# Kernel tuning notes

Hardware: AMD Instinct MI355X
Metric: run time of the kernel (lower is better)

Reference implementation:

```python
import jax, jax.numpy as jnp
import numpy as np

ALPHA = 0.2          # LeakyReLU negative slope
NEG_INF = -9e15      # mask fill value, matches torch source
ADJ_EPS = 1e-6       # clamp min for log(adj)


def setup_inputs() -> dict:
    key = jax.random.key(0)
    k1, k2, k3, k4, k5 = jax.random.split(key, 5)
    N, F_IN, H, D = 4096, 256, 4, 64  # out_features = H*D = 256
    h = jax.random.normal(k1, (N, F_IN), dtype=jnp.float32)
    # xavier_uniform-ish scale for W (gain 1.414)
    limW = 1.414 * np.sqrt(6.0 / (F_IN + D))
    W = jax.random.uniform(k2, (H, F_IN, D), dtype=jnp.float32, minval=-limW, maxval=limW)
    lima = 1.414 * np.sqrt(6.0 / (D + 1))
    a_src = jax.random.uniform(k3, (H, D, 1), dtype=jnp.float32, minval=-lima, maxval=lima)
    a_dst = jax.random.uniform(k4, (H, D, 1), dtype=jnp.float32, minval=-lima, maxval=lima)
    # random 0/1 dense adjacency (float, as the torch module takes log(adj))
    adj = jax.random.randint(k5, (N, N), 0, 2).astype(jnp.float32)
    return {"h": h, "adj": adj, "W": W, "a_src": a_src, "a_dst": a_dst}


def reference(h, adj, W, a_src, a_dst):
    N = h.shape[0]
    # Wh: (H, N, D)
    Wh = jnp.einsum('ni,hid->hnd', h, W)
    # per-node source/dest scores: (H, N, 1)
    attn_src = jnp.einsum('hnd,hdo->hno', Wh, a_src)
    attn_dst = jnp.einsum('hnd,hdo->hno', Wh, a_dst)
    # broadcast to dense (H, N, N) logits
    e = jax.nn.leaky_relu(attn_src + jnp.swapaxes(attn_dst, -1, -2), negative_slope=ALPHA)
    adj_b = adj[None]  # (1, N, N)
    attention = jnp.where(adj_b > 0, e + jnp.log(jnp.maximum(adj_b, ADJ_EPS)), NEG_INF)
    attention = jax.nn.softmax(attention, axis=-1)
    # dropout p=0.0 (eval) -> identity
    h_prime = jnp.einsum('hnm,hmd->hnd', attention, Wh)        # (H, N, D)
    h_prime = jnp.transpose(h_prime, (1, 0, 2)).reshape(N, -1)  # (N, H*D)
    return jax.nn.elu(h_prime)  # concat=True branch
```

## Files before the change

kernel.cpp:

```cpp
#include <hip/hip_runtime.h>

typedef __attribute__((ext_vector_type(4))) float f32x4;
typedef __attribute__((ext_vector_type(8))) short short8;
typedef __attribute__((ext_vector_type(8))) __bf16 bf16x8;

constexpr int kN = 4096;
constexpr int kF = 256;
constexpr int kH = 4;
constexpr int kD = 64;
constexpr int kMP = 264;
constexpr float kLog2e = 1.4426950408889634f;

__device__ __forceinline__ unsigned short f2us(float x) {
  __bf16 b = (__bf16)x;
  return __builtin_bit_cast(unsigned short, b);
}

__global__ __launch_bounds__(256) void k_wh(const float* __restrict__ hmat,
                                            const float* __restrict__ W,
                                            const float* __restrict__ a_src,
                                            const float* __restrict__ a_dst,
                                            unsigned short* __restrict__ whb,
                                            float* __restrict__ s_src,
                                            float* __restrict__ s_dst,
                                            float* __restrict__ pmax) {
  const int h = blockIdx.x & 3, rb = blockIdx.x >> 2;
  const int row0 = rb * 64;
  const int t = threadIdx.x;
  __shared__ unsigned short wlds[16384];
  __shared__ float bm[4];
  {
    const int d = t & 63;
    const int dt = d >> 4, dl = d & 15;
    for (int kb = 0; kb < 64; kb++) {
      const int k = kb * 4 + (t >> 6);
      const float wv = W[((size_t)h * kF + k) * kD + d];
      const int ks = k >> 5, kl = k & 31;
      const int lane2 = ((kl >> 3) << 4) | dl;
      const int e = kl & 7;
      wlds[(((ks * 4 + dt) * 64 + lane2) << 3) + e] = f2us(wv);
    }
  }
  __syncthreads();
  const int wave = t >> 6, lane = t & 63;
  const int lr = lane & 15, lg = lane >> 4;
  const int nrow = row0 + wave * 16 + lr;
  f32x4 acc[4] = {};
  const float* hrow = hmat + (size_t)nrow * kF + 8 * lg;
#pragma unroll
  for (int ks = 0; ks < 8; ks++) {
    const f32x4 h0 = *reinterpret_cast<const f32x4*>(hrow + ks * 32);
    const f32x4 h1 = *reinterpret_cast<const f32x4*>(hrow + ks * 32 + 4);
    bf16x8 af;
#pragma unroll
    for (int j = 0; j < 4; j++) { af[j] = (__bf16)h0[j]; af[4 + j] = (__bf16)h1[j]; }
#pragma unroll
    for (int dt = 0; dt < 4; dt++) {
      const short8 bs = *reinterpret_cast<const short8*>(wlds + (((ks * 4 + dt) * 64 + lane) << 3));
      acc[dt] = __builtin_amdgcn_mfma_f32_16x16x32_bf16(af, __builtin_bit_cast(bf16x8, bs), acc[dt], 0, 0, 0);
    }
  }
#pragma unroll
  for (int dt = 0; dt < 4; dt++) {
#pragma unroll
    for (int r = 0; r < 4; r++) {
      const int n = row0 + wave * 16 + lg * 4 + r;
      const int mstep = n >> 5, kl = n & 31;
      const int lane2 = ((kl >> 3) << 4) | lr;
      const int e = kl & 7;
      whb[((((size_t)(h * 128 + mstep) * 4 + dt) * 64 + lane2) << 3) + e] = f2us(acc[dt][r]);
    }
  }
  float as4[4], ad4[4];
#pragma unroll
  for (int dt = 0; dt < 4; dt++) {
    as4[dt] = a_src[h * kD + dt * 16 + lr];
    ad4[dt] = a_dst[h * kD + dt * 16 + lr];
  }
  float wmax = -1e30f;
#pragma unroll
  for (int r = 0; r < 4; r++) {
    float ps = acc[0][r] * as4[0] + acc[1][r] * as4[1] + acc[2][r] * as4[2] + acc[3][r] * as4[3];
    float pd = acc[0][r] * ad4[0] + acc[1][r] * ad4[1] + acc[2][r] * ad4[2] + acc[3][r] * ad4[3];
#pragma unroll
    for (int off = 1; off < 16; off <<= 1) {
      ps += __shfl_xor(ps, off);
      pd += __shfl_xor(pd, off);
    }
    const int n = row0 + wave * 16 + lg * 4 + r;
    if (lr == 0) { s_src[h * kN + n] = ps; s_dst[h * kN + n] = pd; }
    wmax = fmaxf(wmax, pd);
  }
  wmax = fmaxf(wmax, __shfl_xor(wmax, 16));
  wmax = fmaxf(wmax, __shfl_xor(wmax, 32));
  if (lane == 0) bm[wave] = wmax;
  __syncthreads();
  if (t == 0)
    pmax[blockIdx.x] = fmaxf(fmaxf(bm[0], bm[1]), fmaxf(bm[2], bm[3]));
}

__device__ __forceinline__ bf16x8 make_p2(const f32x4 E1a, const f32x4 E1b,
                                          const f32x4 E2a, const f32x4 E2b,
                                          const float K1, const float K2,
                                          const unsigned int m) {
  bf16x8 r;
#pragma unroll
  for (int j = 0; j < 4; j++) {
    const float pv = fmaxf(E1a[j] * K1, E2a[j] * K2);
    r[j] = (__bf16)((m & (1u << j)) ? pv : 0.0f);
  }
#pragma unroll
  for (int j = 0; j < 4; j++) {
    const float pv = fmaxf(E1b[j] * K1, E2b[j] * K2);
    r[4 + j] = (__bf16)((m & (16u << j)) ? pv : 0.0f);
  }
  return r;
}

__global__ __launch_bounds__(512, 4) void k_attn(const float* __restrict__ adj,
                                                 const unsigned short* __restrict__ whb,
                                                 const float* __restrict__ s_src,
                                                 const float* __restrict__ s_dst,
                                                 const float* __restrict__ pmax,
                                                 float* __restrict__ accP,
                                                 float* __restrict__ zP) {
  const int bid = blockIdx.x;
  const int rb = bid >> 2, cs = bid & 3;
  const int row0 = rb * 32;
  const int colbase = cs * 1024;
  const int t = threadIdx.x;
  const int wave = t >> 6, lane = t & 63;
  const int h = wave & 3, q = wave >> 2;
  const int lr = lane & 15, lg = lane >> 4;

  __shared__ float el1[4][1024];
  __shared__ float el2[4][1024];
  __shared__ unsigned char lmaskB[16 * kMP];
  __shared__ float zx[4][32];

  {
    f32x4 v[16];
    const float* abase = adj + (size_t)(row0 + wave * 4) * kN + colbase;
#pragma unroll
    for (int j = 0; j < 4; j++)
#pragma unroll
      for (int p = 0; p < 4; p++) {
        const int off = ((p >> 1) << 9) + 8 * lane + ((p & 1) << 2);
        v[j * 4 + p] = *reinterpret_cast<const f32x4*>(abase + (size_t)j * kN + off);
      }
#pragma unroll
    for (int j = 0; j < 4; j++) {
      const int rl = wave * 4 + j;
#pragma unroll
      for (int half = 0; half < 2; half++) {
        unsigned int b = 0;
#pragma unroll
        for (int i = 0; i < 4; i++) {
          b |= (v[j * 4 + half * 2][i] != 0.0f ? 1u : 0u) << i;
          b |= (v[j * 4 + half * 2 + 1][i] != 0.0f ? 1u : 0u) << (4 + i);
        }
        const int o = half * 64 + lane;
        lmaskB[(o >> 3) * kMP + rl * 8 + (o & 7)] = (unsigned char)b;
      }
    }
  }

#pragma unroll
  for (int j = 0; j < 2; j++) {
    const int idx = t + j * 512;
    const int hh = idx >> 8, c4 = (idx & 255) * 4;
    const f32x4 sd = *reinterpret_cast<const f32x4*>(s_dst + hh * kN + colbase + c4);
    f32x4 e1, e2;
#pragma unroll
    for (int i = 0; i < 4; i++) {
      const float u = sd[i] * kLog2e;
      e1[i] = __builtin_amdgcn_exp2f(u);
      e2[i] = __builtin_amdgcn_exp2f(0.2f * u);
    }
    *reinterpret_cast<f32x4*>(&el1[hh][c4]) = e1;
    *reinterpret_cast<f32x4*>(&el2[hh][c4]) = e2;
  }

  float M = pmax[(lane << 2) | h];
#pragma unroll
  for (int off = 1; off < 64; off <<= 1) M = fmaxf(M, __shfl_xor(M, off));

  float K1[2], K2[2];
#pragma unroll
  for (int rt = 0; rt < 2; rt++) {
    const float A = s_src[h * kN + row0 + rt * 16 + lr];
    const float xb = A + M;
    const float B = fmaxf(xb, 0.2f * xb);
    K1[rt] = __builtin_amdgcn_exp2f((A - B) * kLog2e);
    K2[rt] = __builtin_amdgcn_exp2f((0.2f * A - B) * kLog2e);
  }

  __syncthreads();

  const int Boff = (q << 2) | lg;
  unsigned int cw0[4], cw1[4];
#pragma unroll
  for (int w = 0; w < 4; w++) {
    unsigned int a0 = 0, a1 = 0;
#pragma unroll
    for (int d = 0; d < 4; d++) {
      const int c = w * 4 + d;
      a0 |= (unsigned int)lmaskB[c * kMP + lr * 8 + Boff] << (8 * d);
      a1 |= (unsigned int)lmaskB[c * kMP + (lr + 16) * 8 + Boff] << (8 * d);
    }
    cw0[w] = a0; cw1[w] = a1;
  }

  f32x4 acc0[4] = {}, acc1[4] = {};
  f32x4 accz0 = {}, accz1 = {};
  bf16x8 ones;
#pragma unroll
  for (int e = 0; e < 8; e++) ones[e] = (__bf16)1.0f;

  const float* e1p = &el1[h][q * 32 + 8 * lg];
  const float* e2p = &el2[h][q * 32 + 8 * lg];
  const short8* wb = reinterpret_cast<const short8*>(whb) + (size_t)h * 32768 + lane;
  const int mstep0 = cs * 32 + q;

  short8 bw[2][4];
#pragma unroll
  for (int s = 0; s < 2; s++) {
    const short8* p = wb + (size_t)(mstep0 + s * 2) * 256;
    bw[s][0] = p[0]; bw[s][1] = p[64]; bw[s][2] = p[128]; bw[s][3] = p[192];
  }

#define UNIT(ITC, CM0, CM1)                                                    \
  {                                                                            \
    const short8 cb0 = bw[(ITC) & 1][0], cb1 = bw[(ITC) & 1][1],               \
                 cb2 = bw[(ITC) & 1][2], cb3 = bw[(ITC) & 1][3];               \
    const short8* pp = wb + (size_t)(mstep0 + ((ITC) + 2) * 2) * 256;          \
    bw[(ITC) & 1][0] = pp[0];                                                  \
    bw[(ITC) & 1][1] = pp[64];                                                 \
    bw[(ITC) & 1][2] = pp[128];                                                \
    bw[(ITC) & 1][3] = pp[192];                                                \
    const f32x4 E1a = *reinterpret_cast<const f32x4*>(e1p + (ITC) * 64);       \
    const f32x4 E1b = *reinterpret_cast<const f32x4*>(e1p + (ITC) * 64 + 4);   \
    const f32x4 E2a = *reinterpret_cast<const f32x4*>(e2p + (ITC) * 64);       \
    const f32x4 E2b = *reinterpret_cast<const f32x4*>(e2p + (ITC) * 64 + 4);   \
    const bf16x8 P0 = make_p2(E1a, E1b, E2a, E2b, K1[0], K2[0], (CM0));        \
    const bf16x8 P1 = make_p2(E1a, E1b, E2a, E2b, K1[1], K2[1], (CM1));        \
    const bf16x8 B0 = __builtin_bit_cast(bf16x8, cb0);                         \
    const bf16x8 B1 = __builtin_bit_cast(bf16x8, cb1);                         \
    const bf16x8 B2 = __builtin_bit_cast(bf16x8, cb2);                         \
    const bf16x8 B3 = __builtin_bit_cast(bf16x8, cb3);                         \
    acc0[0] = __builtin_amdgcn_mfma_f32_16x16x32_bf16(P0, B0, acc0[0], 0, 0, 0); \
    acc1[0] = __builtin_amdgcn_mfma_f32_16x16x32_bf16(P1, B0, acc1[0], 0, 0, 0); \
    acc0[1] = __builtin_amdgcn_mfma_f32_16x16x32_bf16(P0, B1, acc0[1], 0, 0, 0); \
    acc1[1] = __builtin_amdgcn_mfma_f32_16x16x32_bf16(P1, B1, acc1[1], 0, 0, 0); \
    acc0[2] = __builtin_amdgcn_mfma_f32_16x16x32_bf16(P0, B2, acc0[2], 0, 0, 0); \
    acc1[2] = __builtin_amdgcn_mfma_f32_16x16x32_bf16(P1, B2, acc1[2], 0, 0, 0); \
    acc0[3] = __builtin_amdgcn_mfma_f32_16x16x32_bf16(P0, B3, acc0[3], 0, 0, 0); \
    acc1[3] = __builtin_amdgcn_mfma_f32_16x16x32_bf16(P1, B3, acc1[3], 0, 0, 0); \
    accz0 = __builtin_amdgcn_mfma_f32_16x16x32_bf16(P0, ones, accz0, 0, 0, 0); \
    accz1 = __builtin_amdgcn_mfma_f32_16x16x32_bf16(P1, ones, accz1, 0, 0, 0); \
  }

#pragma unroll
  for (int it = 0; it < 16; ++it) {
    const unsigned cm0 = (cw0[it >> 2] >> ((it & 3) * 8)) & 0xFFu;
    const unsigned cm1 = (cw1[it >> 2] >> ((it & 3) * 8)) & 0xFFu;
    UNIT(it, cm0, cm1);
  }
#undef UNIT

  __syncthreads();
  if (q == 1) {
#pragma unroll
    for (int dt = 0; dt < 4; dt++) {
      *reinterpret_cast<f32x4*>(&el1[h][(dt * 64 + lane) * 4]) = acc0[dt];
      *reinterpret_cast<f32x4*>(&el2[h][(dt * 64 + lane) * 4]) = acc1[dt];
    }
    if (lr == 0) {
#pragma unroll
      for (int r = 0; r < 4; r++) {
        zx[h][lg * 4 + r] = accz0[r];
        zx[h][16 + lg * 4 + r] = accz1[r];
      }
    }
  }
  __syncthreads();
  if (q == 0) {
#pragma unroll
    for (int dt = 0; dt < 4; dt++) {
      acc0[dt] += *reinterpret_cast<const f32x4*>(&el1[h][(dt * 64 + lane) * 4]);
      acc1[dt] += *reinterpret_cast<const f32x4*>(&el2[h][(dt * 64 + lane) * 4]);
    }
    const size_t ob = ((size_t)(cs * 4 + h) * kN + row0) * kD;
#pragma unroll
    for (int dt = 0; dt < 4; dt++)
#pragma unroll
      for (int r = 0; r < 4; r++) {
        accP[ob + (size_t)(lg * 4 + r) * kD + dt * 16 + lr] = acc0[dt][r];
        accP[ob + (size_t)(16 + lg * 4 + r) * kD + dt * 16 + lr] = acc1[dt][r];
      }
    if (lr == 0) {
      const size_t zb = (size_t)(cs * 4 + h) * kN + row0;
#pragma unroll
      for (int r = 0; r < 4; r++) {
        zP[zb + lg * 4 + r] = accz0[r] + zx[h][lg * 4 + r];
        zP[zb + 16 + lg * 4 + r] = accz1[r] + zx[h][16 + lg * 4 + r];
      }
    }
  }
}

__global__ __launch_bounds__(256) void k_fin(const float* __restrict__ accP,
                                             const float* __restrict__ zP,
                                             float* __restrict__ out) {
  const int idx = blockIdx.x * 256 + threadIdx.x;
  const int d4 = idx & 15;
  const int hh = (idx >> 4) & 3;
  const int n = idx >> 6;
  f32x4 v = {};
  float z = 0.0f;
#pragma unroll
  for (int s = 0; s < 4; s++) {
    v += reinterpret_cast<const f32x4*>(accP)[((size_t)(s * 4 + hh) * kN + n) * 16 + d4];
    z += zP[(size_t)(s * 4 + hh) * kN + n];
  }
  const float rz = 1.0f / z;
  f32x4 o;
#pragma unroll
  for (int j = 0; j < 4; j++) {
    const float x = v[j] * rz;
    o[j] = x > 0.0f ? x : (__builtin_amdgcn_exp2f(x * kLog2e) - 1.0f);
  }
  reinterpret_cast<f32x4*>(out)[(size_t)n * 64 + hh * 16 + d4] = o;
}

extern "C" void kernel_launch(void* const* d_in, const int* in_sizes, int n_in,
                              void* d_out, int out_size, void* d_ws, size_t ws_size,
                              hipStream_t stream) {
  const float* hmat  = (const float*)d_in[0];
  const float* adj   = (const float*)d_in[1];
  const float* W     = (const float*)d_in[2];
  const float* a_src = (const float*)d_in[3];
  const float* a_dst = (const float*)d_in[4];
  float* out = (float*)d_out;

  char* ws = (char*)d_ws;
  unsigned short* whb = (unsigned short*)(ws);
  float* s_src  = (float*)(ws + 0x200000);
  float* s_dst  = (float*)(ws + 0x210000);
  float* pmax   = (float*)(ws + 0x220000);
  float* accP   = (float*)(ws + 0x240000);
  float* zP     = (float*)(ws + 0x1240000);

  hipLaunchKernelGGL(k_wh, dim3(256), dim3(256), 0, stream,
                     hmat, W, a_src, a_dst, whb, s_src, s_dst, pmax);
  hipLaunchKernelGGL(k_attn, dim3(512), dim3(512), 0, stream,
                     adj, whb, s_src, s_dst, pmax, accP, zP);
  hipLaunchKernelGGL(k_fin, dim3(1024), dim3(256), 0, stream, accP, zP, out);
}
```

Baseline: 51.32 us.

## Split attention column chunk across four wave groups with 1024-thread blocks

Doubles k_attn block size to 1024 threads so each head's 1024-column chunk is split across four wave groups instead of two. Each wave does half the MFMA iterations, adj mask loading is spread over more waves, and partial accumulators are combined through an extra two-level LDS reduction. It also replaces the conditional mask select with a bitwise AND mask. This adds shared memory (an extra 32KB buffer), more barriers and register-pressure limits under launch_bounds(1024,8), in exchange for more latency hiding per CU.

Result: slower. 121.6 us (+137.0%).

```diff
diff --git a/kernel.cpp b/kernel.cpp
--- a/kernel.cpp
+++ b/kernel.cpp
@@ -99,31 +99,32 @@
     pmax[blockIdx.x] = fmaxf(fmaxf(bm[0], bm[1]), fmaxf(bm[2], bm[3]));
 }
 
+__device__ __forceinline__ float msel(float pv, unsigned m, int j) {
+  const unsigned keep = (unsigned)(-(int)((m >> j) & 1u));
+  return __builtin_bit_cast(float, __builtin_bit_cast(unsigned, pv) & keep);
+}
+
 __device__ __forceinline__ bf16x8 make_p2(const f32x4 E1a, const f32x4 E1b,
                                           const f32x4 E2a, const f32x4 E2b,
                                           const float K1, const float K2,
                                           const unsigned int m) {
   bf16x8 r;
 #pragma unroll
-  for (int j = 0; j < 4; j++) {
-    const float pv = fmaxf(E1a[j] * K1, E2a[j] * K2);
-    r[j] = (__bf16)((m & (1u << j)) ? pv : 0.0f);
-  }
-#pragma unroll
-  for (int j = 0; j < 4; j++) {
-    const float pv = fmaxf(E1b[j] * K1, E2b[j] * K2);
-    r[4 + j] = (__bf16)((m & (16u << j)) ? pv : 0.0f);
-  }
+  for (int j = 0; j < 4; j++)
+    r[j] = (__bf16)msel(fmaxf(E1a[j] * K1, E2a[j] * K2), m, j);
+#pragma unroll
+  for (int j = 0; j < 4; j++)
+    r[4 + j] = (__bf16)msel(fmaxf(E1b[j] * K1, E2b[j] * K2), m, 4 + j);
   return r;
 }
 
-__global__ __launch_bounds__(512, 4) void k_attn(const float* __restrict__ adj,
-                                                 const unsigned short* __restrict__ whb,
-                                                 const float* __restrict__ s_src,
-                                                 const float* __restrict__ s_dst,
-                                                 const float* __restrict__ pmax,
-                                                 float* __restrict__ accP,
-                                                 float* __restrict__ zP) {
+__global__ __launch_bounds__(1024, 8) void k_attn(const float* __restrict__ adj,
+                                                  const unsigned short* __restrict__ whb,
+                                                  const float* __restrict__ s_src,
+                                                  const float* __restrict__ s_dst,
+                                                  const float* __restrict__ pmax,
+                                                  float* __restrict__ accP,
+                                                  float* __restrict__ zP) {
   const int bid = blockIdx.x;
   const int rb = bid >> 2, cs = bid & 3;
   const int row0 = rb * 32;
@@ -135,22 +136,23 @@
 
   __shared__ float el1[4][1024];
   __shared__ float el2[4][1024];
+  __shared__ float cb2[4][2048];
   __shared__ unsigned char lmaskB[16 * kMP];
-  __shared__ float zx[4][32];
+  __shared__ float zxA[4][32], zxB[4][32];
 
   {
-    f32x4 v[16];
-    const float* abase = adj + (size_t)(row0 + wave * 4) * kN + colbase;
-#pragma unroll
-    for (int j = 0; j < 4; j++)
+    f32x4 v[8];
+    const float* abase = adj + (size_t)(row0 + wave * 2) * kN + colbase;
+#pragma unroll
+    for (int j = 0; j < 2; j++)
 #pragma unroll
       for (int p = 0; p < 4; p++) {
         const int off = ((p >> 1) << 9) + 8 * lane + ((p & 1) << 2);
         v[j * 4 + p] = *reinterpret_cast<const f32x4*>(abase + (size_t)j * kN + off);
       }
 #pragma unroll
-    for (int j = 0; j < 4; j++) {
-      const int rl = wave * 4 + j;
+    for (int j = 0; j < 2; j++) {
+      const int rl = wave * 2 + j;
 #pragma unroll
       for (int half = 0; half < 2; half++) {
         unsigned int b = 0;
@@ -165,10 +167,8 @@
     }
   }
 
-#pragma unroll
-  for (int j = 0; j < 2; j++) {
-    const int idx = t + j * 512;
-    const int hh = idx >> 8, c4 = (idx & 255) * 4;
+  {
+    const int hh = t >> 8, c4 = (t & 255) * 4;
     const f32x4 sd = *reinterpret_cast<const f32x4*>(s_dst + hh * kN + colbase + c4);
     f32x4 e1, e2;
 #pragma unroll
@@ -197,19 +197,17 @@
 
   __syncthreads();
 
-  const int Boff = (q << 2) | lg;
-  unsigned int cw0[4], cw1[4];
-#pragma unroll
-  for (int w = 0; w < 4; w++) {
-    unsigned int a0 = 0, a1 = 0;
+  const int g = 4 * q + lg;
+  const int base_c = g >> 3, s = g & 7;
+  unsigned int cw0[2] = {0, 0}, cw1[2] = {0, 0};
+#pragma unroll
+  for (int w = 0; w < 2; w++)
 #pragma unroll
     for (int d = 0; d < 4; d++) {
-      const int c = w * 4 + d;
-      a0 |= (unsigned int)lmaskB[c * kMP + lr * 8 + Boff] << (8 * d);
-      a1 |= (unsigned int)lmaskB[c * kMP + (lr + 16) * 8 + Boff] << (8 * d);
-    }
-    cw0[w] = a0; cw1[w] = a1;
-  }
+      const int c = base_c + 8 * w + 2 * d;
+      cw0[w] |= (unsigned int)lmaskB[c * kMP + lr * 8 + s] << (8 * d);
+      cw1[w] |= (unsigned int)lmaskB[c * kMP + (lr + 16) * 8 + s] << (8 * d);
+    }
 
   f32x4 acc0[4] = {}, acc1[4] = {};
   f32x4 accz0 = {}, accz1 = {};
@@ -224,29 +222,29 @@
 
   short8 bw[2][4];
 #pragma unroll
-  for (int s = 0; s < 2; s++) {
-    const short8* p = wb + (size_t)(mstep0 + s * 2) * 256;
-    bw[s][0] = p[0]; bw[s][1] = p[64]; bw[s][2] = p[128]; bw[s][3] = p[192];
+  for (int sx = 0; sx < 2; sx++) {
+    const short8* p = wb + (size_t)(mstep0 + sx * 4) * 256;
+    bw[sx][0] = p[0]; bw[sx][1] = p[64]; bw[sx][2] = p[128]; bw[sx][3] = p[192];
   }
 
 #define UNIT(ITC, CM0, CM1)                                                    \
   {                                                                            \
     const short8 cb0 = bw[(ITC) & 1][0], cb1 = bw[(ITC) & 1][1],               \
-                 cb2 = bw[(ITC) & 1][2], cb3 = bw[(ITC) & 1][3];               \
-    const short8* pp = wb + (size_t)(mstep0 + ((ITC) + 2) * 2) * 256;          \
+                 cb2r = bw[(ITC) & 1][2], cb3 = bw[(ITC) & 1][3];              \
+    const short8* pp = wb + (size_t)(mstep0 + ((ITC) + 2) * 4) * 256;          \
     bw[(ITC) & 1][0] = pp[0];                                                  \
     bw[(ITC) & 1][1] = pp[64];                                                 \
     bw[(ITC) & 1][2] = pp[128];                                                \
     bw[(ITC) & 1][3] = pp[192];                                                \
-    const f32x4 E1a = *reinterpret_cast<const f32x4*>(e1p + (ITC) * 64);       \
-    const f32x4 E1b = *reinterpret_cast<const f32x4*>(e1p + (ITC) * 64 + 4);   \
-    const f32x4 E2a = *reinterpret_cast<const f32x4*>(e2p + (ITC) * 64);       \
-    const f32x4 E2b = *reinterpret_cast<const f32x4*>(e2p + (ITC) * 64 + 4);   \
+    const f32x4 E1a = *reinterpret_cast<const f32x4*>(e1p + (ITC) * 128);      \
+    const f32x4 E1b = *reinterpret_cast<const f32x4*>(e1p + (ITC) * 128 + 4);  \
+    const f32x4 E2a = *reinterpret_cast<const f32x4*>(e2p + (ITC) * 128);      \
+    const f32x4 E2b = *reinterpret_cast<const f32x4*>(e2p + (ITC) * 128 + 4);  \
     const bf16x8 P0 = make_p2(E1a, E1b, E2a, E2b, K1[0], K2[0], (CM0));        \
     const bf16x8 P1 = make_p2(E1a, E1b, E2a, E2b, K1[1], K2[1], (CM1));        \
     const bf16x8 B0 = __builtin_bit_cast(bf16x8, cb0);                         \
     const bf16x8 B1 = __builtin_bit_cast(bf16x8, cb1);                         \
-    const bf16x8 B2 = __builtin_bit_cast(bf16x8, cb2);                         \
+    const bf16x8 B2 = __builtin_bit_cast(bf16x8, cb2r);                        \
     const bf16x8 B3 = __builtin_bit_cast(bf16x8, cb3);                         \
     acc0[0] = __builtin_amdgcn_mfma_f32_16x16x32_bf16(P0, B0, acc0[0], 0, 0, 0); \
     acc1[0] = __builtin_amdgcn_mfma_f32_16x16x32_bf16(P1, B0, acc1[0], 0, 0, 0); \
@@ -261,7 +259,7 @@
   }
 
 #pragma unroll
-  for (int it = 0; it < 16; ++it) {
+  for (int it = 0; it < 8; ++it) {
     const unsigned cm0 = (cw0[it >> 2] >> ((it & 3) * 8)) & 0xFFu;
     const unsigned cm1 = (cw1[it >> 2] >> ((it & 3) * 8)) & 0xFFu;
     UNIT(it, cm0, cm1);
@@ -275,13 +273,59 @@
       *reinterpret_cast<f32x4*>(&el1[h][(dt * 64 + lane) * 4]) = acc0[dt];
       *reinterpret_cast<f32x4*>(&el2[h][(dt * 64 + lane) * 4]) = acc1[dt];
     }
-    if (lr == 0) {
+    if (lr == 0)
 #pragma unroll
       for (int r = 0; r < 4; r++) {
-        zx[h][lg * 4 + r] = accz0[r];
-        zx[h][16 + lg * 4 + r] = accz1[r];
-      }
-    }
+        zxA[h][lg * 4 + r] = accz0[r];
+        zxA[h][16 + lg * 4 + r] = accz1[r];
+      }
+  }
+  if (q == 3) {
+#pragma unroll
+    for (int dt = 0; dt < 4; dt++) {
+      *reinterpret_cast<f32x4*>(&cb2[h][(dt * 64 + lane) * 4]) = acc0[dt];
+      *reinterpret_cast<f32x4*>(&cb2[h][1024 + (dt * 64 + lane) * 4]) = acc1[dt];
+    }
+    if (lr == 0)
+#pragma unroll
+      for (int r = 0; r < 4; r++) {
+        zxB[h][lg * 4 + r] = accz0[r];
+        zxB[h][16 + lg * 4 + r] = accz1[r];
+      }
+  }
+  __syncthreads();
+  if (q == 0) {
+#pragma unroll
+    for (int dt = 0; dt < 4; dt++) {
+      acc0[dt] += *reinterpret_cast<const f32x4*>(&el1[h][(dt * 64 + lane) * 4]);
+      acc1[dt] += *reinterpret_cast<const f32x4*>(&el2[h][(dt * 64 + lane) * 4]);
+    }
+  }
+  if (q == 2) {
+#pragma unroll
+    for (int dt = 0; dt < 4; dt++) {
+      acc0[dt] += *reinterpret_cast<const f32x4*>(&cb2[h][(dt * 64 + lane) * 4]);
+      acc1[dt] += *reinterpret_cast<const f32x4*>(&cb2[h][1024 + (dt * 64 + lane) * 4]);
+    }
+#pragma unroll
+    for (int r = 0; r < 4; r++) {
+      accz0[r] += zxB[h][lg * 4 + r];
+      accz1[r] += zxB[h][16 + lg * 4 + r];
+    }
+  }
+  __syncthreads();
+  if (q == 2) {
+#pragma unroll
+    for (int dt = 0; dt < 4; dt++) {
+      *reinterpret_cast<f32x4*>(&el1[h][(dt * 64 + lane) * 4]) = acc0[dt];
+      *reinterpret_cast<f32x4*>(&el2[h][(dt * 64 + lane) * 4]) = acc1[dt];
+    }
+    if (lr == 0)
+#pragma unroll
+      for (int r = 0; r < 4; r++) {
+        zxB[h][lg * 4 + r] = accz0[r];
+        zxB[h][16 + lg * 4 + r] = accz1[r];
+      }
   }
   __syncthreads();
   if (q == 0) {
@@ -302,8 +346,9 @@
       const size_t zb = (size_t)(cs * 4 + h) * kN + row0;
 #pragma unroll
       for (int r = 0; r < 4; r++) {
-        zP[zb + lg * 4 + r] = accz0[r] + zx[h][lg * 4 + r];
-        zP[zb + 16 + lg * 4 + r] = accz1[r] + zx[h][16 + lg * 4 + r];
+        zP[zb + lg * 4 + r] = accz0[r] + zxA[h][lg * 4 + r] + zxB[h][lg * 4 + r];
+        zP[zb + 16 + lg * 4 + r] =
+            accz1[r] + zxA[h][16 + lg * 4 + r] + zxB[h][16 + lg * 4 + r];
       }
     }
   }
@@ -353,7 +398,7 @@
 
   hipLaunchKernelGGL(k_wh, dim3(256), dim3(256), 0, stream,
                      hmat, W, a_src, a_dst, whb, s_src, s_dst, pmax);
-  hipLaunchKernelGGL(k_attn, dim3(512), dim3(512), 0, stream,
+  hipLaunchKernelGGL(k_attn, dim3(512), dim3(1024), 0, stream,
                      adj, whb, s_src, s_dst, pmax, accP, zP);
   hipLaunchKernelGGL(k_fin, dim3(1024), dim3(256), 0, stream, accP, zP, out);
 }
```

## Halve attention row tile to 16 rows, double grid and raise occupancy

Applied to the files above, without the earlier changes.

The attention kernel now handles 16 query rows per block instead of 32 and launches 1024 blocks instead of 512, with launch bounds asking for 8 blocks per CU. The mask-row layout and the second accumulator set are dropped to match. The masked select now uses a bitwise AND with a sign-extended mask bit instead of a conditional. The aim is more parallelism and occupancy to hide memory latency, at the cost of loading Wh and computing the exp tables twice as often per row, since each B fragment now feeds one P tile instead of two.

After: 53.03 us. 1.03x slower.

```diff
diff --git a/kernel.cpp b/kernel.cpp
--- a/kernel.cpp
+++ b/kernel.cpp
@@ -8,7 +8,7 @@
 constexpr int kF = 256;
 constexpr int kH = 4;
 constexpr int kD = 64;
-constexpr int kMP = 264;
+constexpr int kMP = 136;
 constexpr float kLog2e = 1.4426950408889634f;
 
 __device__ __forceinline__ unsigned short f2us(float x) {
@@ -99,25 +99,26 @@
     pmax[blockIdx.x] = fmaxf(fmaxf(bm[0], bm[1]), fmaxf(bm[2], bm[3]));
 }
 
+__device__ __forceinline__ float msel(float pv, unsigned m, int j) {
+  const unsigned keep = (unsigned)(-(int)((m >> j) & 1u));
+  return __builtin_bit_cast(float, __builtin_bit_cast(unsigned, pv) & keep);
+}
+
 __device__ __forceinline__ bf16x8 make_p2(const f32x4 E1a, const f32x4 E1b,
                                           const f32x4 E2a, const f32x4 E2b,
                                           const float K1, const float K2,
                                           const unsigned int m) {
   bf16x8 r;
 #pragma unroll
-  for (int j = 0; j < 4; j++) {
-    const float pv = fmaxf(E1a[j] * K1, E2a[j] * K2);
-    r[j] = (__bf16)((m & (1u << j)) ? pv : 0.0f);
-  }
-#pragma unroll
-  for (int j = 0; j < 4; j++) {
-    const float pv = fmaxf(E1b[j] * K1, E2b[j] * K2);
-    r[4 + j] = (__bf16)((m & (16u << j)) ? pv : 0.0f);
-  }
+  for (int j = 0; j < 4; j++)
+    r[j] = (__bf16)msel(fmaxf(E1a[j] * K1, E2a[j] * K2), m, j);
+#pragma unroll
+  for (int j = 0; j < 4; j++)
+    r[4 + j] = (__bf16)msel(fmaxf(E1b[j] * K1, E2b[j] * K2), m, 4 + j);
   return r;
 }
 
-__global__ __launch_bounds__(512, 4) void k_attn(const float* __restrict__ adj,
+__global__ __launch_bounds__(512, 8) void k_attn(const float* __restrict__ adj,
                                                  const unsigned short* __restrict__ whb,
                                                  const float* __restrict__ s_src,
                                                  const float* __restrict__ s_dst,
@@ -126,7 +127,7 @@
                                                  float* __restrict__ zP) {
   const int bid = blockIdx.x;
   const int rb = bid >> 2, cs = bid & 3;
-  const int row0 = rb * 32;
+  const int row0 = rb * 16;
   const int colbase = cs * 1024;
   const int t = threadIdx.x;
   const int wave = t >> 6, lane = t & 63;
@@ -136,21 +137,21 @@
   __shared__ float el1[4][1024];
   __shared__ float el2[4][1024];
   __shared__ unsigned char lmaskB[16 * kMP];
-  __shared__ float zx[4][32];
+  __shared__ float zx[4][16];
 
   {
-    f32x4 v[16];
-    const float* abase = adj + (size_t)(row0 + wave * 4) * kN + colbase;
-#pragma unroll
-    for (int j = 0; j < 4; j++)
+    f32x4 v[8];
+    const float* abase = adj + (size_t)(row0 + wave * 2) * kN + colbase;
+#pragma unroll
+    for (int j = 0; j < 2; j++)
 #pragma unroll
       for (int p = 0; p < 4; p++) {
         const int off = ((p >> 1) << 9) + 8 * lane + ((p & 1) << 2);
         v[j * 4 + p] = *reinterpret_cast<const f32x4*>(abase + (size_t)j * kN + off);
       }
 #pragma unroll
-    for (int j = 0; j < 4; j++) {
-      const int rl = wave * 4 + j;
+    for (int j = 0; j < 2; j++) {
+      const int rl = wave * 2 + j;
 #pragma unroll
       for (int half = 0; half < 2; half++) {
         unsigned int b = 0;
@@ -159,8 +160,7 @@
           b |= (v[j * 4 + half * 2][i] != 0.0f ? 1u : 0u) << i;
           b |= (v[j * 4 + half * 2 + 1][i] != 0.0f ? 1u : 0u) << (4 + i);
         }
-        const int o = half * 64 + lane;
-        lmaskB[(o >> 3) * kMP + rl * 8 + (o & 7)] = (unsigned char)b;
+        lmaskB[(half * 8 + (lane >> 3)) * kMP + rl * 8 + (lane & 7)] = (unsigned char)b;
       }
     }
   }
@@ -185,34 +185,24 @@
 #pragma unroll
   for (int off = 1; off < 64; off <<= 1) M = fmaxf(M, __shfl_xor(M, off));
 
-  float K1[2], K2[2];
-#pragma unroll
-  for (int rt = 0; rt < 2; rt++) {
-    const float A = s_src[h * kN + row0 + rt * 16 + lr];
-    const float xb = A + M;
-    const float B = fmaxf(xb, 0.2f * xb);
-    K1[rt] = __builtin_amdgcn_exp2f((A - B) * kLog2e);
-    K2[rt] = __builtin_amdgcn_exp2f((0.2f * A - B) * kLog2e);
-  }
-
-  __syncthreads();
-
-  const int Boff = (q << 2) | lg;
-  unsigned int cw0[4], cw1[4];
-#pragma unroll
-  for (int w = 0; w < 4; w++) {
-    unsigned int a0 = 0, a1 = 0;
-#pragma unroll
-    for (int d = 0; d < 4; d++) {
-      const int c = w * 4 + d;
-      a0 |= (unsigned int)lmaskB[c * kMP + lr * 8 + Boff] << (8 * d);
-      a1 |= (unsigned int)lmaskB[c * kMP + (lr + 16) * 8 + Boff] << (8 * d);
-    }
-    cw0[w] = a0; cw1[w] = a1;
-  }
-
-  f32x4 acc0[4] = {}, acc1[4] = {};
-  f32x4 accz0 = {}, accz1 = {};
+  const float A = s_src[h * kN + row0 + lr];
+  const float xb = A + M;
+  const float B = fmaxf(xb, 0.2f * xb);
+  const float K1 = __builtin_amdgcn_exp2f((A - B) * kLog2e);
+  const float K2 = __builtin_amdgcn_exp2f((0.2f * A - B) * kLog2e);
+
+  __syncthreads();
+
+  const int s = (q << 2) | lg;
+  unsigned int cw[4] = {0, 0, 0, 0};
+#pragma unroll
+  for (int w = 0; w < 4; w++)
+#pragma unroll
+    for (int d = 0; d < 4; d++)
+      cw[w] |= (unsigned int)lmaskB[(w * 4 + d) * kMP + lr * 8 + s] << (8 * d);
+
+  f32x4 acc[4] = {};
+  f32x4 accz = {};
   bf16x8 ones;
 #pragma unroll
   for (int e = 0; e < 8; e++) ones[e] = (__bf16)1.0f;
@@ -224,12 +214,12 @@
 
   short8 bw[2][4];
 #pragma unroll
-  for (int s = 0; s < 2; s++) {
-    const short8* p = wb + (size_t)(mstep0 + s * 2) * 256;
-    bw[s][0] = p[0]; bw[s][1] = p[64]; bw[s][2] = p[128]; bw[s][3] = p[192];
-  }
-
-#define UNIT(ITC, CM0, CM1)                                                    \
+  for (int sx = 0; sx < 2; sx++) {
+    const short8* p = wb + (size_t)(mstep0 + sx * 2) * 256;
+    bw[sx][0] = p[0]; bw[sx][1] = p[64]; bw[sx][2] = p[128]; bw[sx][3] = p[192];
+  }
+
+#define UNIT(ITC, CM)                                                          \
   {                                                                            \
     const short8 cb0 = bw[(ITC) & 1][0], cb1 = bw[(ITC) & 1][1],               \
                  cb2 = bw[(ITC) & 1][2], cb3 = bw[(ITC) & 1][3];               \
@@ -242,69 +232,50 @@
     const f32x4 E1b = *reinterpret_cast<const f32x4*>(e1p + (ITC) * 64 + 4);   \
     const f32x4 E2a = *reinterpret_cast<const f32x4*>(e2p + (ITC) * 64);       \
     const f32x4 E2b = *reinterpret_cast<const f32x4*>(e2p + (ITC) * 64 + 4);   \
-    const bf16x8 P0 = make_p2(E1a, E1b, E2a, E2b, K1[0], K2[0], (CM0));        \
-    const bf16x8 P1 = make_p2(E1a, E1b, E2a, E2b, K1[1], K2[1], (CM1));        \
-    const bf16x8 B0 = __builtin_bit_cast(bf16x8, cb0);                         \
-    const bf16x8 B1 = __builtin_bit_cast(bf16x8, cb1);                         \
-    const bf16x8 B2 = __builtin_bit_cast(bf16x8, cb2);                         \
-    const bf16x8 B3 = __builtin_bit_cast(bf16x8, cb3);                         \
-    acc0[0] = __builtin_amdgcn_mfma_f32_16x16x32_bf16(P0, B0, acc0[0], 0, 0, 0); \
-    acc1[0] = __builtin_amdgcn_mfma_f32_16x16x32_bf16(P1, B0, acc1[0], 0, 0, 0); \
-    acc0[1] = __builtin_amdgcn_mfma_f32_16x16x32_bf16(P0, B1, acc0[1], 0, 0, 0); \
-    acc1[1] = __builtin_amdgcn_mfma_f32_16x16x32_bf16(P1, B1, acc1[1], 0, 0, 0); \
-    acc0[2] = __builtin_amdgcn_mfma_f32_16x16x32_bf16(P0, B2, acc0[2], 0, 0, 0); \
-    acc1[2] = __builtin_amdgcn_mfma_f32_16x16x32_bf16(P1, B2, acc1[2], 0, 0, 0); \
-    acc0[3] = __builtin_amdgcn_mfma_f32_16x16x32_bf16(P0, B3, acc0[3], 0, 0, 0); \
-    acc1[3] = __builtin_amdgcn_mfma_f32_16x16x32_bf16(P1, B3, acc1[3], 0, 0, 0); \
-    accz0 = __builtin_amdgcn_mfma_f32_16x16x32_bf16(P0, ones, accz0, 0, 0, 0); \
-    accz1 = __builtin_amdgcn_mfma_f32_16x16x32_bf16(P1, ones, accz1, 0, 0, 0); \
+    const bf16x8 P0 = make_p2(E1a, E1b, E2a, E2b, K1, K2, (CM));               \
+    acc[0] = __builtin_amdgcn_mfma_f32_16x16x32_bf16(                          \
+        P0, __builtin_bit_cast(bf16x8, cb0), acc[0], 0, 0, 0);                 \
+    acc[1] = __builtin_amdgcn_mfma_f32_16x16x32_bf16(                          \
+        P0, __builtin_bit_cast(bf16x8, cb1), acc[1], 0, 0, 0);                 \
+    acc[2] = __builtin_amdgcn_mfma_f32_16x16x32_bf16(                          \
+        P0, __builtin_bit_cast(bf16x8, cb2), acc[2], 0, 0, 0);                 \
+    acc[3] = __builtin_amdgcn_mfma_f32_16x16x32_bf16(                          \
+        P0, __builtin_bit_cast(bf16x8, cb3), acc[3], 0, 0, 0);                 \
+    accz = __builtin_amdgcn_mfma_f32_16x16x32_bf16(P0, ones, accz, 0, 0, 0);   \
   }
 
 #pragma unroll
   for (int it = 0; it < 16; ++it) {
-    const unsigned cm0 = (cw0[it >> 2] >> ((it & 3) * 8)) & 0xFFu;
-    const unsigned cm1 = (cw1[it >> 2] >> ((it & 3) * 8)) & 0xFFu;
-    UNIT(it, cm0, cm1);
+    const unsigned cm = (cw[it >> 2] >> ((it & 3) * 8)) & 0xFFu;
+    UNIT(it, cm);
   }
 #undef UNIT
 
   __syncthreads();
   if (q == 1) {
 #pragma unroll
-    for (int dt = 0; dt < 4; dt++) {
-      *reinterpret_cast<f32x4*>(&el1[h][(dt * 64 + lane) * 4]) = acc0[dt];
-      *reinterpret_cast<f32x4*>(&el2[h][(dt * 64 + lane) * 4]) = acc1[dt];
-    }
+    for (int dt = 0; dt < 4; dt++)
+      *reinterpret_cast<f32x4*>(&el1[h][(dt * 64 + lane) * 4]) = acc[dt];
+    if (lr == 0)
+#pragma unroll
+      for (int r = 0; r < 4; r++) zx[h][lg * 4 + r] = accz[r];
+  }
+  __syncthreads();
+  if (q == 0) {
+#pragma unroll
+    for (int dt = 0; dt < 4; dt++)
+      acc[dt] += *reinterpret_cast<const f32x4*>(&el1[h][(dt * 64 + lane) * 4]);
+
+    const size_t ob = ((size_t)(cs * 4 + h) * kN + row0) * kD;
+#pragma unroll
+    for (int dt = 0; dt < 4; dt++)
+#pragma unroll
+      for (int r = 0; r < 4; r++)
+        accP[ob + (size_t)(lg * 4 + r) * kD + dt * 16 + lr] = acc[dt][r];
     if (lr == 0) {
 #pragma unroll
-      for (int r = 0; r < 4; r++) {
-        zx[h][lg * 4 + r] = accz0[r];
-        zx[h][16 + lg * 4 + r] = accz1[r];
-      }
-    }
-  }
-  __syncthreads();
-  if (q == 0) {
-#pragma unroll
-    for (int dt = 0; dt < 4; dt++) {
-      acc0[dt] += *reinterpret_cast<const f32x4*>(&el1[h][(dt * 64 + lane) * 4]);
-      acc1[dt] += *reinterpret_cast<const f32x4*>(&el2[h][(dt * 64 + lane) * 4]);
-    }
-    const size_t ob = ((size_t)(cs * 4 + h) * kN + row0) * kD;
-#pragma unroll
-    for (int dt = 0; dt < 4; dt++)
-#pragma unroll
-      for (int r = 0; r < 4; r++) {
-        accP[ob + (size_t)(lg * 4 + r) * kD + dt * 16 + lr] = acc0[dt][r];
-        accP[ob + (size_t)(16 + lg * 4 + r) * kD + dt * 16 + lr] = acc1[dt][r];
-      }
-    if (lr == 0) {
-      const size_t zb = (size_t)(cs * 4 + h) * kN + row0;
-#pragma unroll
-      for (int r = 0; r < 4; r++) {
-        zP[zb + lg * 4 + r] = accz0[r] + zx[h][lg * 4 + r];
-        zP[zb + 16 + lg * 4 + r] = accz1[r] + zx[h][16 + lg * 4 + r];
-      }
+      for (int r = 0; r < 4; r++)
+        zP[(size_t)(cs * 4 + h) * kN + row0 + lg * 4 + r] = accz[r] + zx[h][lg * 4 + r];
     }
   }
 }
@@ -353,7 +324,7 @@
 
   hipLaunchKernelGGL(k_wh, dim3(256), dim3(256), 0, stream,
                      hmat, W, a_src, a_dst, whb, s_src, s_dst, pmax);
-  hipLaunchKernelGGL(k_attn, dim3(512), dim3(512), 0, stream,
+  hipLaunchKernelGGL(k_attn, dim3(1024), dim3(512), 0, stream,
                      adj, whb, s_src, s_dst, pmax, accP, zP);
   hipLaunchKernelGGL(k_fin, dim3(1024), dim3(256), 0, stream, accP, zP, out);
 }
```
